# Optimization experiments

Hardware: AMD Instinct MI355X
Metric: run time of the kernel (lower is better)

## Reference

```python
import jax, jax.numpy as jnp
import numpy as np

N_NODES = 50000
N_GRAPHS = 2048
BN_EPS = 1e-5


def setup_inputs() -> dict:
    key = jax.random.key(0)
    ks = jax.random.split(key, 12)
    n_feat, dim, n_out, n_edges = 128, 128, 12, 800000
    x = jax.random.normal(ks[0], (N_NODES, n_feat), dtype=jnp.float32)
    edge_index = jax.random.randint(ks[1], (2, n_edges), 0, N_NODES, dtype=jnp.int32)
    batch = jnp.sort(jax.random.randint(ks[2], (N_NODES,), 0, N_GRAPHS, dtype=jnp.int32))
    def lin(k, fan_in, fan_out):
        bound = 1.0 / np.sqrt(fan_in)
        kw, kb = jax.random.split(k)
        W = jax.random.uniform(kw, (fan_in, fan_out), minval=-bound, maxval=bound, dtype=jnp.float32)
        b = jax.random.uniform(kb, (fan_out,), minval=-bound, maxval=bound, dtype=jnp.float32)
        return W, b
    W1, b1 = lin(ks[3], n_feat, dim)
    W2, b2 = lin(ks[4], dim, dim)
    gamma = jnp.ones((dim,), dtype=jnp.float32)
    beta = jnp.zeros((dim,), dtype=jnp.float32)
    Wf1, bf1 = lin(ks[5], dim, 2 * dim)
    Wf2, bf2 = lin(ks[6], 2 * dim, n_out)
    return {"x": x, "edge_index": edge_index, "batch": batch,
            "W1": W1, "b1": b1, "W2": W2, "b2": b2,
            "gamma": gamma, "beta": beta,
            "Wf1": Wf1, "bf1": bf1, "Wf2": Wf2, "bf2": bf2}


def reference(x, edge_index, batch, W1, b1, W2, b2, gamma, beta, Wf1, bf1, Wf2, bf2):
    src, dst = edge_index[0], edge_index[1]
    # GINConv (eps=0): h = nn1(x + sum_{j in N(i)} x_j), scatter-add at dst
    agg = jax.ops.segment_sum(x[src], dst, num_segments=N_NODES)  # [N, F]
    h = x + agg
    h = jax.nn.relu(h @ W1 + b1) @ W2 + b2  # nn1 MLP
    h = jax.nn.relu(h)
    # BatchNorm1d (training mode: batch statistics, biased variance)
    mean = jnp.mean(h, axis=0)
    var = jnp.mean((h - mean) ** 2, axis=0)
    h = (h - mean) * jax.lax.rsqrt(var + BN_EPS) * gamma + beta
    # global_add_pool over graphs
    g = jax.ops.segment_sum(h, batch, num_segments=N_GRAPHS)  # [G, dim]
    g = jax.nn.relu(g @ Wf1 + bf1)
    return g @ Wf2 + bf2  # [G, n_outputs]
```

## Files before the change

kernel.cpp:

```cpp
#include <hip/hip_runtime.h>

#define N_FEAT   128
#define N_GRAPHS 2048
#define BN_EPS   1e-5f
#define LDA      136
#define FHLD     132
#define EPB      4096

typedef __attribute__((ext_vector_type(8))) short  bf16x8;
typedef __attribute__((ext_vector_type(4))) float  f32x4;

__device__ __forceinline__ unsigned short f2bf(float f) {
    union { float f; unsigned int u; } c; c.f = f;
    unsigned int r = c.u + 0x7fffu + ((c.u >> 16) & 1u);
    return (unsigned short)(r >> 16);
}
__device__ __forceinline__ float bf2f(unsigned short h) {
    union { unsigned int u; float f; } c; c.u = ((unsigned int)h) << 16;
    return c.f;
}

__device__ __forceinline__ void acc8(float* a, int4 u) {
    unsigned int w[4] = {(unsigned int)u.x, (unsigned int)u.y,
                         (unsigned int)u.z, (unsigned int)u.w};
    #pragma unroll
    for (int k = 0; k < 4; ++k) {
        a[2 * k]     += __uint_as_float(w[k] << 16);
        a[2 * k + 1] += __uint_as_float(w[k] & 0xffff0000u);
    }
}

__global__ __launch_bounds__(256) void k_prep(const float* __restrict__ x,
                                              unsigned short* __restrict__ xb,
                                              int n8, int nbx,
                                              const float* __restrict__ W1,
                                              const float* __restrict__ W2,
                                              unsigned short* __restrict__ Wt1,
                                              unsigned short* __restrict__ Wt2,
                                              const int* __restrict__ batch,
                                              int* __restrict__ cnt, int n_nodes)
{
    int b = blockIdx.x, t = threadIdx.x;
    if (b < nbx) {
        int i = b * 256 + t;
        if (i >= n8) return;
        float4 a = ((const float4*)x)[i * 2];
        float4 c = ((const float4*)x)[i * 2 + 1];
        ushort4 u0, u1;
        u0.x = f2bf(a.x); u0.y = f2bf(a.y); u0.z = f2bf(a.z); u0.w = f2bf(a.w);
        u1.x = f2bf(c.x); u1.y = f2bf(c.y); u1.z = f2bf(c.z); u1.w = f2bf(c.w);
        ((ushort4*)xb)[i * 2]     = u0;
        ((ushort4*)xb)[i * 2 + 1] = u1;
    } else if (b < nbx + 128) {
        int i = (b - nbx) * 256 + t;
        int which = i >> 14;
        int k = (i >> 7) & 127;
        int c = i & 127;
        const float* W = which ? W2 : W1;
        unsigned short* O = which ? Wt2 : Wt1;
        O[c * 128 + k] = f2bf(W[k * 128 + c]);
    } else {
        int i = (b - nbx - 128) * 256 + t;
        if (i < n_nodes) atomicAdd(&cnt[batch[i]], 1);
    }
}

__global__ __launch_bounds__(256) void k_bhist(const int* __restrict__ dst,
                                               int* __restrict__ bcnt,
                                               int n_edges, int nb2)
{
    __shared__ int lc[256];
    int t = threadIdx.x;
    lc[t] = 0;
    __syncthreads();
    int base = blockIdx.x * EPB;
    for (int i = t; i < EPB; i += 256) {
        int e = base + i;
        if (e < n_edges) atomicAdd(&lc[dst[e] >> 8], 1);
    }
    __syncthreads();
    bcnt[t * nb2 + blockIdx.x] = lc[t];
}

__global__ __launch_bounds__(256) void k_bsum(const int* __restrict__ v,
                                              int* __restrict__ chsum, int n)
{
    __shared__ int s[256];
    int t = threadIdx.x;
    int i = blockIdx.x * 256 + t;
    s[t] = (i < n) ? v[i] : 0;
    __syncthreads();
    for (int o = 128; o > 0; o >>= 1) {
        if (t < o) s[t] += s[t + o];
        __syncthreads();
    }
    if (t == 0) chsum[blockIdx.x] = s[0];
}

__global__ __launch_bounds__(1024) void k_bscan2(const int* __restrict__ chsum,
                                                 int* __restrict__ choff, int nchunk)
{
    __shared__ int s[1024];
    int t = threadIdx.x;
    int v = (t < nchunk) ? chsum[t] : 0;
    s[t] = v;
    __syncthreads();
    for (int o = 1; o < 1024; o <<= 1) {
        int u = (t >= o) ? s[t - o] : 0;
        __syncthreads();
        s[t] += u;
        __syncthreads();
    }
    choff[t] = s[t] - v;
}

__global__ __launch_bounds__(256) void k_bapply(const int* __restrict__ v,
                                                const int* __restrict__ choff,
                                                int* __restrict__ out, int n)
{
    __shared__ int s[256];
    int t = threadIdx.x;
    int i = blockIdx.x * 256 + t;
    int c = (i < n) ? v[i] : 0;
    s[t] = c;
    __syncthreads();
    for (int o = 1; o < 256; o <<= 1) {
        int u = (t >= o) ? s[t - o] : 0;
        __syncthreads();
        s[t] += u;
        __syncthreads();
    }
    if (i < n) out[i] = choff[blockIdx.x] + s[t] - c;
}

__global__ __launch_bounds__(256) void k_part(const int* __restrict__ src,
                                              const int* __restrict__ dst,
                                              const int* __restrict__ boff2,
                                              unsigned* __restrict__ epart,
                                              int n_edges, int nb2)
{
    __shared__ int lc[256];
    __shared__ int lofs[256];
    __shared__ unsigned buf[EPB];
    int t = threadIdx.x, blk = blockIdx.x;
    int base = blk * EPB;
    lc[t] = 0;
    __syncthreads();
    for (int i = t; i < EPB; i += 256) {
        int e = base + i;
        if (e < n_edges) atomicAdd(&lc[dst[e] >> 8], 1);
    }
    __syncthreads();
    int v = lc[t];
    lofs[t] = v;
    __syncthreads();
    for (int o = 1; o < 256; o <<= 1) {
        int u = (t >= o) ? lofs[t - o] : 0;
        __syncthreads();
        lofs[t] += u;
        __syncthreads();
    }
    int excl = lofs[t] - v;
    __syncthreads();
    lofs[t] = excl;
    lc[t] = 0;
    __syncthreads();
    for (int i = t; i < EPB; i += 256) {
        int e = base + i;
        if (e < n_edges) {
            int d = dst[e];
            int b = d >> 8;
            unsigned pack = ((unsigned)d << 16) | (unsigned)src[e];
            int r = atomicAdd(&lc[b], 1);
            buf[lofs[b] + r] = pack;
        }
    }
    __syncthreads();
    int total = min(EPB, n_edges - base);
    for (int i = t; i < total; i += 256) {
        unsigned pack = buf[i];
        int b = pack >> 24;
        int gpos = boff2[b * nb2 + blk] + (i - lofs[b]);
        epart[gpos] = pack;
    }
}

__global__ __launch_bounds__(256) void k_bfill(const unsigned* __restrict__ epart,
                                               const int* __restrict__ boff2,
                                               int* __restrict__ row_start,
                                               unsigned short* __restrict__ csr,
                                               int n_nodes, int nb2, int nbkt)
{
    __shared__ int cur[256];
    __shared__ int sc2[256];
    __shared__ unsigned short seg[8192];
    int t = threadIdx.x, b = blockIdx.x;
    int node0 = b * 256;
    int nodes = min(256, n_nodes - node0);
    int ebeg = boff2[(size_t)b * nb2];
    int eend = (b + 1 < nbkt) ? boff2[(size_t)(b + 1) * nb2] : boff2[(size_t)nbkt * nb2];

    cur[t] = 0;
    __syncthreads();
    for (int i = ebeg + t; i < eend; i += 256)
        atomicAdd(&cur[(epart[i] >> 16) - node0], 1);
    __syncthreads();
    int v = cur[t];
    sc2[t] = v;
    __syncthreads();
    for (int o = 1; o < 256; o <<= 1) {
        int u = (t >= o) ? sc2[t - o] : 0;
        __syncthreads();
        sc2[t] += u;
        __syncthreads();
    }
    int excl = sc2[t] - v;
    if (t < nodes) row_start[node0 + t] = ebeg + excl;
    if (b == nbkt - 1 && t == 0) row_start[n_nodes] = eend;
    __syncthreads();
    cur[t] = excl;
    __syncthreads();
    for (int i = ebeg + t; i < eend; i += 256) {
        unsigned pack = epart[i];
        int idx = (pack >> 16) - node0;
        int slot = atomicAdd(&cur[idx], 1);
        seg[slot] = (unsigned short)(pack & 0xffffu);
    }
    __syncthreads();
    int seglen = eend - ebeg;
    for (int i = t; i < seglen; i += 256) csr[ebeg + i] = seg[i];
}

__global__ __launch_bounds__(256) void k_gather(const float* __restrict__ x,
                                                const unsigned short* __restrict__ xb,
                                                const unsigned short* __restrict__ csr,
                                                const int* __restrict__ row_start,
                                                unsigned short* __restrict__ Ahi,
                                                unsigned short* __restrict__ Alo,
                                                int n_nodes)
{
    int node = blockIdx.x * 4 + (threadIdx.x >> 6);
    if (node >= n_nodes) return;
    int l = threadIdx.x & 63;
    int q = l >> 4;
    int lq = l & 15;
    const int4* xb4 = (const int4*)xb;
    int beg = row_start[node], end = row_start[node + 1];
    float a[8];
    #pragma unroll
    for (int i = 0; i < 8; ++i) a[i] = 0.f;

    int j = beg + q;
    for (; j + 4 < end; j += 8) {
        int s0 = csr[j], s1 = csr[j + 4];
        int4 u0 = xb4[(size_t)s0 * 16 + lq];
        int4 u1 = xb4[(size_t)s1 * 16 + lq];
        acc8(a, u0);
        acc8(a, u1);
    }
    for (; j < end; j += 4) {
        int4 u = xb4[(size_t)csr[j] * 16 + lq];
        acc8(a, u);
    }
    #pragma unroll
    for (int i = 0; i < 8; ++i) {
        a[i] += __shfl_xor(a[i], 16);
        a[i] += __shfl_xor(a[i], 32);
    }
    if (q == 0) {
        float4 s0 = ((const float4*)(x + (size_t)node * 128))[lq * 2];
        float4 s1 = ((const float4*)(x + (size_t)node * 128))[lq * 2 + 1];
        a[0] += s0.x; a[1] += s0.y; a[2] += s0.z; a[3] += s0.w;
        a[4] += s1.x; a[5] += s1.y; a[6] += s1.z; a[7] += s1.w;
        unsigned int hw[4], lw[4];
        #pragma unroll
        for (int i = 0; i < 4; ++i) {
            unsigned short h0 = f2bf(a[2 * i]);
            unsigned short h1 = f2bf(a[2 * i + 1]);
            unsigned short l0 = f2bf(a[2 * i] - bf2f(h0));
            unsigned short l1 = f2bf(a[2 * i + 1] - bf2f(h1));
            hw[i] = (unsigned int)h0 | ((unsigned int)h1 << 16);
            lw[i] = (unsigned int)l0 | ((unsigned int)l1 << 16);
        }
        int4 hv = make_int4(hw[0], hw[1], hw[2], hw[3]);
        int4 lv = make_int4(lw[0], lw[1], lw[2], lw[3]);
        *(int4*)(Ahi + (size_t)node * 128 + lq * 8) = hv;
        *(int4*)(Alo + (size_t)node * 128 + lq * 8) = lv;
    }
}

__global__ __launch_bounds__(256) void k_mlp1_mfma(const unsigned short* __restrict__ Ahi,
                                                   const unsigned short* __restrict__ Alo,
                                                   const unsigned short* __restrict__ Wt1,
                                                   const float* __restrict__ b1,
                                                   const unsigned short* __restrict__ Wt2,
                                                   const float* __restrict__ b2,
                                                   const int* __restrict__ batch,
                                                   float* __restrict__ g_raw,
                                                   float* __restrict__ partial,
                                                   int n_rows)
{
    __shared__ __align__(16) char smem[64 * LDA * 2 * sizeof(unsigned short)];
    unsigned short* sHi = (unsigned short*)smem;
    unsigned short* sLo = sHi + 64 * LDA;

    int t = threadIdx.x;
    int wave = t >> 6, l = t & 63;
    int lr = l & 15;
    int lk = l >> 4;
    int row0 = blockIdx.x * 64;
    int col0 = wave * 32;

    #pragma unroll
    for (int it = 0; it < 4; ++it) {
        int idx = it * 256 + t;
        int r = idx >> 4, c8 = idx & 15;
        int gr = row0 + r;
        int4 vh = make_int4(0, 0, 0, 0), vl = make_int4(0, 0, 0, 0);
        if (gr < n_rows) {
            vh = ((const int4*)(Ahi + (size_t)gr * 128))[c8];
            vl = ((const int4*)(Alo + (size_t)gr * 128))[c8];
        }
        *(int4*)&sHi[r * LDA + c8 * 8] = vh;
        *(int4*)&sLo[r * LDA + c8 * 8] = vl;
    }
    __syncthreads();

    f32x4 acc[4][2];
    #pragma unroll
    for (int m = 0; m < 4; ++m)
        #pragma unroll
        for (int n = 0; n < 2; ++n) acc[m][n] = (f32x4){0.f, 0.f, 0.f, 0.f};

    #pragma unroll
    for (int ks = 0; ks < 4; ++ks) {
        bf16x8 bfrag[2];
        #pragma unroll
        for (int n = 0; n < 2; ++n) {
            int c = col0 + n * 16 + lr;
            bfrag[n] = *(const bf16x8*)(Wt1 + (size_t)c * 128 + ks * 32 + lk * 8);
        }
        #pragma unroll
        for (int m = 0; m < 4; ++m) {
            bf16x8 ah = *(const bf16x8*)&sHi[(m * 16 + lr) * LDA + ks * 32 + lk * 8];
            bf16x8 al = *(const bf16x8*)&sLo[(m * 16 + lr) * LDA + ks * 32 + lk * 8];
            #pragma unroll
            for (int n = 0; n < 2; ++n) {
                acc[m][n] = __builtin_amdgcn_mfma_f32_16x16x32_bf16(ah, bfrag[n], acc[m][n], 0, 0, 0);
                acc[m][n] = __builtin_amdgcn_mfma_f32_16x16x32_bf16(al, bfrag[n], acc[m][n], 0, 0, 0);
            }
        }
    }
    __syncthreads();

    #pragma unroll
    for (int n = 0; n < 2; ++n) {
        int c = col0 + n * 16 + lr;
        float bb = b1[c];
        #pragma unroll
        for (int m = 0; m < 4; ++m) {
            #pragma unroll
            for (int i = 0; i < 4; ++i) {
                int r = m * 16 + lk * 4 + i;
                float v = fmaxf(acc[m][n][i] + bb, 0.f);
                unsigned short hb = f2bf(v);
                sHi[r * LDA + c] = hb;
                sLo[r * LDA + c] = f2bf(v - bf2f(hb));
            }
        }
    }
    __syncthreads();

    #pragma unroll
    for (int m = 0; m < 4; ++m)
        #pragma unroll
        for (int n = 0; n < 2; ++n) acc[m][n] = (f32x4){0.f, 0.f, 0.f, 0.f};

    #pragma unroll
    for (int ks = 0; ks < 4; ++ks) {
        bf16x8 bfrag[2];
        #pragma unroll
        for (int n = 0; n < 2; ++n) {
            int c = col0 + n * 16 + lr;
            bfrag[n] = *(const bf16x8*)(Wt2 + (size_t)c * 128 + ks * 32 + lk * 8);
        }
        #pragma unroll
        for (int m = 0; m < 4; ++m) {
            bf16x8 ah = *(const bf16x8*)&sHi[(m * 16 + lr) * LDA + ks * 32 + lk * 8];
            bf16x8 al = *(const bf16x8*)&sLo[(m * 16 + lr) * LDA + ks * 32 + lk * 8];
            #pragma unroll
            for (int n = 0; n < 2; ++n) {
                acc[m][n] = __builtin_amdgcn_mfma_f32_16x16x32_bf16(ah, bfrag[n], acc[m][n], 0, 0, 0);
                acc[m][n] = __builtin_amdgcn_mfma_f32_16x16x32_bf16(al, bfrag[n], acc[m][n], 0, 0, 0);
            }
        }
    }

    float bb0 = b2[col0 + lr];
    float bb1 = b2[col0 + 16 + lr];
    int c0 = col0 + lr, c1 = col0 + 16 + lr;
    float v0s[4][4], v1s[4][4];
    float ps[2] = {0.f, 0.f}, pq[2] = {0.f, 0.f};
    #pragma unroll
    for (int m = 0; m < 4; ++m) {
        #pragma unroll
        for (int i = 0; i < 4; ++i) {
            int gr = row0 + m * 16 + lk * 4 + i;
            float v0 = fmaxf(acc[m][0][i] + bb0, 0.f);
            float v1 = fmaxf(acc[m][1][i] + bb1, 0.f);
            if (gr >= n_rows) { v0 = 0.f; v1 = 0.f; }
            v0s[m][i] = v0; v1s[m][i] = v1;
            ps[0] += v0; pq[0] += v0 * v0;
            ps[1] += v1; pq[1] += v1 * v1;
        }
    }
    #pragma unroll
    for (int n = 0; n < 2; ++n) {
        ps[n] += __shfl_xor(ps[n], 16); ps[n] += __shfl_xor(ps[n], 32);
        pq[n] += __shfl_xor(pq[n], 16); pq[n] += __shfl_xor(pq[n], 32);
    }
    if (lk == 0) {
        partial[(size_t)blockIdx.x * 256 + c0]       = ps[0];
        partial[(size_t)blockIdx.x * 256 + c1]       = ps[1];
        partial[(size_t)blockIdx.x * 256 + 128 + c0] = pq[0];
        partial[(size_t)blockIdx.x * 256 + 128 + c1] = pq[1];
    }

    __syncthreads();
    float (*fH)[FHLD] = (float (*)[FHLD])smem;
    int* sB = (int*)(smem + 64 * FHLD * sizeof(float));
    if (t < 64) sB[t] = (row0 + t < n_rows) ? batch[row0 + t] : -1;
    #pragma unroll
    for (int m = 0; m < 4; ++m) {
        #pragma unroll
        for (int i = 0; i < 4; ++i) {
            int r = m * 16 + lk * 4 + i;
            fH[r][c0] = v0s[m][i];
            fH[r][c1] = v1s[m][i];
        }
    }
    __syncthreads();

    {
        int c = t & 127;
        int rbeg = (t >> 7) * 32, rend = rbeg + 32;
        float a = 0.f;
        int bcur = sB[rbeg];
        for (int r = rbeg; r < rend; ++r) {
            int b = sB[r];
            if (b != bcur) {
                if (bcur >= 0) unsafeAtomicAdd(&g_raw[(size_t)bcur * 128 + c], a);
                a = 0.f; bcur = b;
            }
            a += fH[r][c];
        }
        if (bcur >= 0) unsafeAtomicAdd(&g_raw[(size_t)bcur * 128 + c], a);
    }
}

__global__ __launch_bounds__(256) void k_bnred(const float* __restrict__ partial,
                                               float* __restrict__ stats, int nblk)
{
    int j = threadIdx.x;
    float s = 0.f;
    for (int b = blockIdx.x; b < nblk; b += gridDim.x)
        s += partial[(size_t)b * 256 + j];
    unsafeAtomicAdd(&stats[j], s);
}

__global__ __launch_bounds__(256) void k_head(const float* __restrict__ g_raw,
                                              const int* __restrict__ cnt,
                                              const float* __restrict__ stats,
                                              const float* __restrict__ gamma,
                                              const float* __restrict__ beta,
                                              const float* __restrict__ Wf1,
                                              const float* __restrict__ bf1,
                                              const float* __restrict__ Wf2,
                                              const float* __restrict__ bf2,
                                              float* __restrict__ out, int n_rows)
{
    __shared__ float sg[128];
    __shared__ float sh[256];
    int t = threadIdx.x;
    int G = blockIdx.x;
    if (t < 128) {
        float inv_n = 1.0f / (float)n_rows;
        float mean = stats[t] * inv_n;
        float var = stats[128 + t] * inv_n - mean * mean;
        float inv = rsqrtf(var + BN_EPS);
        float scale = gamma[t] * inv;
        float shift = beta[t] - mean * scale;
        float c = (float)cnt[G];
        sg[t] = g_raw[(size_t)G * 128 + t] * scale + c * shift;
    }
    __syncthreads();
    float a = bf1[t];
    #pragma unroll 8
    for (int k = 0; k < 128; ++k) a = fmaf(sg[k], Wf1[k * 256 + t], a);
    sh[t] = fmaxf(a, 0.f);
    __syncthreads();
    if (t < 192) {
        int o = t >> 4, l = t & 15;
        float p = 0.f;
        for (int k = l; k < 256; k += 16) p += sh[k] * Wf2[k * 12 + o];
        #pragma unroll
        for (int m = 8; m >= 1; m >>= 1) p += __shfl_xor(p, m, 16);
        if (l == 0) out[(size_t)G * 12 + o] = p + bf2[o];
    }
}

extern "C" void kernel_launch(void* const* d_in, const int* in_sizes, int n_in,
                              void* d_out, int out_size, void* d_ws, size_t ws_size,
                              hipStream_t stream)
{
    const float* x     = (const float*)d_in[0];
    const int*   ei    = (const int*)d_in[1];
    const int*   batch = (const int*)d_in[2];
    const float* W1    = (const float*)d_in[3];
    const float* b1    = (const float*)d_in[4];
    const float* W2    = (const float*)d_in[5];
    const float* b2    = (const float*)d_in[6];
    const float* gamma = (const float*)d_in[7];
    const float* beta  = (const float*)d_in[8];
    const float* Wf1   = (const float*)d_in[9];
    const float* bf1   = (const float*)d_in[10];
    const float* Wf2   = (const float*)d_in[11];
    const float* bf2   = (const float*)d_in[12];

    int n_nodes = in_sizes[0] / N_FEAT;
    int n_edges = in_sizes[1] / 2;
    const int* src = ei;
    const int* dst = ei + n_edges;

    char* ws = (char*)d_ws;
    size_t planeBytes = (size_t)n_nodes * N_FEAT * sizeof(unsigned short);
    size_t gBytes     = (size_t)N_GRAPHS * N_FEAT * sizeof(float);
    int nblk_m = (n_nodes + 63) / 64;
    int nb2    = (n_edges + EPB - 1) / EPB;
    int nbkt   = (n_nodes + 255) / 256;
    int nscan  = 256 * nb2;
    int nchunk = (nscan + 255) / 256;

    unsigned short* Ahi = (unsigned short*)ws;
    unsigned short* Alo = (unsigned short*)(ws + planeBytes);
    unsigned short* xb  = (unsigned short*)(ws + 2 * planeBytes);
    float* g_raw = (float*)(ws + 3 * planeBytes);
    float* stats = (float*)((char*)g_raw + gBytes);
    float* sc    = stats + 256;
    int*   cnt   = (int*)(sc + 256);
    unsigned short* Wt1 = (unsigned short*)(cnt + N_GRAPHS);
    unsigned short* Wt2 = Wt1 + 128 * 128;
    float* partial = (float*)(Wt2 + 128 * 128);
    char* p = (char*)(partial + (size_t)nblk_m * 256);
    int* row_start = (int*)p;   p += (size_t)(n_nodes + 1) * sizeof(int);
    int* bcnt      = (int*)p;   p += (size_t)nscan * sizeof(int);
    int* bch       = (int*)p;   p += 1024 * sizeof(int);
    int* bchoff    = (int*)p;   p += 1024 * sizeof(int);
    int* boff2     = (int*)p;   p += (size_t)nscan * sizeof(int);
    unsigned* epart = (unsigned*)p;  p += (size_t)n_edges * sizeof(unsigned);
    unsigned short* csr = (unsigned short*)p;

    hipMemsetAsync(g_raw, 0, gBytes + (256 + 256 + N_GRAPHS) * sizeof(float), stream);

    int n8 = n_nodes * N_FEAT / 8;
    int nbx = (n8 + 255) / 256;
    int nbg = (n_nodes + 255) / 256;
    k_prep<<<nbx + 128 + nbg, 256, 0, stream>>>(x, xb, n8, nbx, W1, W2, Wt1, Wt2,
                                                batch, cnt, n_nodes);

    k_bhist<<<nb2, 256, 0, stream>>>(dst, bcnt, n_edges, nb2);
    k_bsum<<<nchunk, 256, 0, stream>>>(bcnt, bch, nscan);
    k_bscan2<<<1, 1024, 0, stream>>>(bch, bchoff, nchunk);
    k_bapply<<<nchunk, 256, 0, stream>>>(bcnt, bchoff, boff2, nscan);
    k_part<<<nb2, 256, 0, stream>>>(src, dst, boff2, epart, n_edges, nb2);
    k_bfill<<<nbkt, 256, 0, stream>>>(epart, boff2, row_start, csr, n_nodes, nb2, nbkt);

    k_gather<<<(n_nodes + 3) / 4, 256, 0, stream>>>(x, xb, csr, row_start, Ahi, Alo, n_nodes);

    k_mlp1_mfma<<<nblk_m, 256, 0, stream>>>(Ahi, Alo, Wt1, b1, Wt2, b2, batch,
                                            g_raw, partial, n_nodes);

    k_bnred<<<64, 256, 0, stream>>>(partial, stats, nblk_m);
    k_head<<<N_GRAPHS, 256, 0, stream>>>(g_raw, cnt, stats, gamma, beta,
                                         Wf1, bf1, Wf2, bf2, (float*)d_out, n_nodes);
}
```

Before: 135.9 us.

## Drop bf16 hi/lo split in MLP and fuse bucket scan into two kernels

The MLP stage no longer splits activations into high and low bf16 planes. It keeps one bf16 plane, which halves the MFMA count, the LDS traffic and the gather stores. The three-kernel bucket prefix scan becomes per-bucket totals accumulated atomically in the histogram kernel plus a single scan kernel, removing two launches. The precision loss on activations could push the output beyond tolerance, and the new scan assumes nb2 is at most 256.

New measurement: 129.8 us. 1.05x faster.

```diff
diff --git a/kernel.cpp b/kernel.cpp
--- a/kernel.cpp
+++ b/kernel.cpp
@@ -67,6 +67,7 @@
 
 __global__ __launch_bounds__(256) void k_bhist(const int* __restrict__ dst,
                                                int* __restrict__ bcnt,
+                                               int* __restrict__ btot,
                                                int n_edges, int nb2)
 {
     __shared__ int lc[256];
@@ -80,48 +81,24 @@
     }
     __syncthreads();
     bcnt[t * nb2 + blockIdx.x] = lc[t];
-}
-
-__global__ __launch_bounds__(256) void k_bsum(const int* __restrict__ v,
-                                              int* __restrict__ chsum, int n)
+    if (lc[t]) atomicAdd(&btot[t], lc[t]);
+}
+
+__global__ __launch_bounds__(256) void k_bscan3(const int* __restrict__ bcnt,
+                                                const int* __restrict__ btot,
+                                                int* __restrict__ boff2, int nb2)
 {
     __shared__ int s[256];
-    int t = threadIdx.x;
-    int i = blockIdx.x * 256 + t;
-    s[t] = (i < n) ? v[i] : 0;
+    int t = threadIdx.x, b = blockIdx.x;
+    s[t] = (t < b) ? btot[t] : 0;
     __syncthreads();
     for (int o = 128; o > 0; o >>= 1) {
         if (t < o) s[t] += s[t + o];
         __syncthreads();
     }
-    if (t == 0) chsum[blockIdx.x] = s[0];
-}
-
-__global__ __launch_bounds__(1024) void k_bscan2(const int* __restrict__ chsum,
-                                                 int* __restrict__ choff, int nchunk)
-{
-    __shared__ int s[1024];
-    int t = threadIdx.x;
-    int v = (t < nchunk) ? chsum[t] : 0;
-    s[t] = v;
-    __syncthreads();
-    for (int o = 1; o < 1024; o <<= 1) {
-        int u = (t >= o) ? s[t - o] : 0;
-        __syncthreads();
-        s[t] += u;
-        __syncthreads();
-    }
-    choff[t] = s[t] - v;
-}
-
-__global__ __launch_bounds__(256) void k_bapply(const int* __restrict__ v,
-                                                const int* __restrict__ choff,
-                                                int* __restrict__ out, int n)
-{
-    __shared__ int s[256];
-    int t = threadIdx.x;
-    int i = blockIdx.x * 256 + t;
-    int c = (i < n) ? v[i] : 0;
+    int base = s[0];
+    __syncthreads();
+    int c = (t < nb2) ? bcnt[b * nb2 + t] : 0;
     s[t] = c;
     __syncthreads();
     for (int o = 1; o < 256; o <<= 1) {
@@ -130,7 +107,7 @@
         s[t] += u;
         __syncthreads();
     }
-    if (i < n) out[i] = choff[blockIdx.x] + s[t] - c;
+    if (t < nb2) boff2[b * nb2 + t] = base + s[t] - c;
 }
 
 __global__ __launch_bounds__(256) void k_part(const int* __restrict__ src,
@@ -235,8 +212,7 @@
                                                 const unsigned short* __restrict__ xb,
                                                 const unsigned short* __restrict__ csr,
                                                 const int* __restrict__ row_start,
-                                                unsigned short* __restrict__ Ahi,
-                                                unsigned short* __restrict__ Alo,
+                                                unsigned short* __restrict__ A,
                                                 int n_nodes)
 {
     int node = blockIdx.x * 4 + (threadIdx.x >> 6);
@@ -272,25 +248,18 @@
         float4 s1 = ((const float4*)(x + (size_t)node * 128))[lq * 2 + 1];
         a[0] += s0.x; a[1] += s0.y; a[2] += s0.z; a[3] += s0.w;
         a[4] += s1.x; a[5] += s1.y; a[6] += s1.z; a[7] += s1.w;
-        unsigned int hw[4], lw[4];
+        unsigned int hw[4];
         #pragma unroll
         for (int i = 0; i < 4; ++i) {
             unsigned short h0 = f2bf(a[2 * i]);
             unsigned short h1 = f2bf(a[2 * i + 1]);
-            unsigned short l0 = f2bf(a[2 * i] - bf2f(h0));
-            unsigned short l1 = f2bf(a[2 * i + 1] - bf2f(h1));
             hw[i] = (unsigned int)h0 | ((unsigned int)h1 << 16);
-            lw[i] = (unsigned int)l0 | ((unsigned int)l1 << 16);
-        }
-        int4 hv = make_int4(hw[0], hw[1], hw[2], hw[3]);
-        int4 lv = make_int4(lw[0], lw[1], lw[2], lw[3]);
-        *(int4*)(Ahi + (size_t)node * 128 + lq * 8) = hv;
-        *(int4*)(Alo + (size_t)node * 128 + lq * 8) = lv;
-    }
-}
-
-__global__ __launch_bounds__(256) void k_mlp1_mfma(const unsigned short* __restrict__ Ahi,
-                                                   const unsigned short* __restrict__ Alo,
+        }
+        *(int4*)(A + (size_t)node * 128 + lq * 8) = make_int4(hw[0], hw[1], hw[2], hw[3]);
+    }
+}
+
+__global__ __launch_bounds__(256) void k_mlp1_mfma(const unsigned short* __restrict__ A,
                                                    const unsigned short* __restrict__ Wt1,
                                                    const float* __restrict__ b1,
                                                    const unsigned short* __restrict__ Wt2,
@@ -300,9 +269,8 @@
                                                    float* __restrict__ partial,
                                                    int n_rows)
 {
-    __shared__ __align__(16) char smem[64 * LDA * 2 * sizeof(unsigned short)];
-    unsigned short* sHi = (unsigned short*)smem;
-    unsigned short* sLo = sHi + 64 * LDA;
+    __shared__ __align__(16) char smem[64 * FHLD * 4 + 256];
+    unsigned short* sA = (unsigned short*)smem;
 
     int t = threadIdx.x;
     int wave = t >> 6, l = t & 63;
@@ -316,13 +284,9 @@
         int idx = it * 256 + t;
         int r = idx >> 4, c8 = idx & 15;
         int gr = row0 + r;
-        int4 vh = make_int4(0, 0, 0, 0), vl = make_int4(0, 0, 0, 0);
-        if (gr < n_rows) {
-            vh = ((const int4*)(Ahi + (size_t)gr * 128))[c8];
-            vl = ((const int4*)(Alo + (size_t)gr * 128))[c8];
-        }
-        *(int4*)&sHi[r * LDA + c8 * 8] = vh;
-        *(int4*)&sLo[r * LDA + c8 * 8] = vl;
+        int4 vh = make_int4(0, 0, 0, 0);
+        if (gr < n_rows) vh = ((const int4*)(A + (size_t)gr * 128))[c8];
+        *(int4*)&sA[r * LDA + c8 * 8] = vh;
     }
     __syncthreads();
 
@@ -342,13 +306,10 @@
         }
         #pragma unroll
         for (int m = 0; m < 4; ++m) {
-            bf16x8 ah = *(const bf16x8*)&sHi[(m * 16 + lr) * LDA + ks * 32 + lk * 8];
-            bf16x8 al = *(const bf16x8*)&sLo[(m * 16 + lr) * LDA + ks * 32 + lk * 8];
+            bf16x8 ah = *(const bf16x8*)&sA[(m * 16 + lr) * LDA + ks * 32 + lk * 8];
             #pragma unroll
-            for (int n = 0; n < 2; ++n) {
+            for (int n = 0; n < 2; ++n)
                 acc[m][n] = __builtin_amdgcn_mfma_f32_16x16x32_bf16(ah, bfrag[n], acc[m][n], 0, 0, 0);
-                acc[m][n] = __builtin_amdgcn_mfma_f32_16x16x32_bf16(al, bfrag[n], acc[m][n], 0, 0, 0);
-            }
         }
     }
     __syncthreads();
@@ -362,10 +323,7 @@
             #pragma unroll
             for (int i = 0; i < 4; ++i) {
                 int r = m * 16 + lk * 4 + i;
-                float v = fmaxf(acc[m][n][i] + bb, 0.f);
-                unsigned short hb = f2bf(v);
-                sHi[r * LDA + c] = hb;
-                sLo[r * LDA + c] = f2bf(v - bf2f(hb));
+                sA[r * LDA + c] = f2bf(fmaxf(acc[m][n][i] + bb, 0.f));
             }
         }
     }
@@ -386,13 +344,10 @@
         }
         #pragma unroll
         for (int m = 0; m < 4; ++m) {
-            bf16x8 ah = *(const bf16x8*)&sHi[(m * 16 + lr) * LDA + ks * 32 + lk * 8];
-            bf16x8 al = *(const bf16x8*)&sLo[(m * 16 + lr) * LDA + ks * 32 + lk * 8];
+            bf16x8 ah = *(const bf16x8*)&sA[(m * 16 + lr) * LDA + ks * 32 + lk * 8];
             #pragma unroll
-            for (int n = 0; n < 2; ++n) {
+            for (int n = 0; n < 2; ++n)
                 acc[m][n] = __builtin_amdgcn_mfma_f32_16x16x32_bf16(ah, bfrag[n], acc[m][n], 0, 0, 0);
-                acc[m][n] = __builtin_amdgcn_mfma_f32_16x16x32_bf16(al, bfrag[n], acc[m][n], 0, 0, 0);
-            }
         }
     }
 
@@ -539,28 +494,25 @@
     int nb2    = (n_edges + EPB - 1) / EPB;
     int nbkt   = (n_nodes + 255) / 256;
     int nscan  = 256 * nb2;
-    int nchunk = (nscan + 255) / 256;
-
-    unsigned short* Ahi = (unsigned short*)ws;
-    unsigned short* Alo = (unsigned short*)(ws + planeBytes);
-    unsigned short* xb  = (unsigned short*)(ws + 2 * planeBytes);
-    float* g_raw = (float*)(ws + 3 * planeBytes);
+
+    unsigned short* A   = (unsigned short*)ws;
+    unsigned short* xb  = (unsigned short*)(ws + planeBytes);
+    float* g_raw = (float*)(ws + 2 * planeBytes);
     float* stats = (float*)((char*)g_raw + gBytes);
-    float* sc    = stats + 256;
-    int*   cnt   = (int*)(sc + 256);
-    unsigned short* Wt1 = (unsigned short*)(cnt + N_GRAPHS);
+    float* scSp  = stats + 256;
+    int*   cnt   = (int*)(scSp + 256);
+    int*   btot  = cnt + N_GRAPHS;
+    unsigned short* Wt1 = (unsigned short*)(btot + 256);
     unsigned short* Wt2 = Wt1 + 128 * 128;
     float* partial = (float*)(Wt2 + 128 * 128);
     char* p = (char*)(partial + (size_t)nblk_m * 256);
     int* row_start = (int*)p;   p += (size_t)(n_nodes + 1) * sizeof(int);
     int* bcnt      = (int*)p;   p += (size_t)nscan * sizeof(int);
-    int* bch       = (int*)p;   p += 1024 * sizeof(int);
-    int* bchoff    = (int*)p;   p += 1024 * sizeof(int);
     int* boff2     = (int*)p;   p += (size_t)nscan * sizeof(int);
     unsigned* epart = (unsigned*)p;  p += (size_t)n_edges * sizeof(unsigned);
     unsigned short* csr = (unsigned short*)p;
 
-    hipMemsetAsync(g_raw, 0, gBytes + (256 + 256 + N_GRAPHS) * sizeof(float), stream);
+    hipMemsetAsync(g_raw, 0, gBytes + (256 + 256 + N_GRAPHS + 256) * sizeof(float), stream);
 
     int n8 = n_nodes * N_FEAT / 8;
     int nbx = (n8 + 255) / 256;
@@ -568,16 +520,14 @@
     k_prep<<<nbx + 128 + nbg, 256, 0, stream>>>(x, xb, n8, nbx, W1, W2, Wt1, Wt2,
                                                 batch, cnt, n_nodes);
 
-    k_bhist<<<nb2, 256, 0, stream>>>(dst, bcnt, n_edges, nb2);
-    k_bsum<<<nchunk, 256, 0, stream>>>(bcnt, bch, nscan);
-    k_bscan2<<<1, 1024, 0, stream>>>(bch, bchoff, nchunk);
-    k_bapply<<<nchunk, 256, 0, stream>>>(bcnt, bchoff, boff2, nscan);
+    k_bhist<<<nb2, 256, 0, stream>>>(dst, bcnt, btot, n_edges, nb2);
+    k_bscan3<<<256, 256, 0, stream>>>(bcnt, btot, boff2, nb2);
     k_part<<<nb2, 256, 0, stream>>>(src, dst, boff2, epart, n_edges, nb2);
     k_bfill<<<nbkt, 256, 0, stream>>>(epart, boff2, row_start, csr, n_nodes, nb2, nbkt);
 
-    k_gather<<<(n_nodes + 3) / 4, 256, 0, stream>>>(x, xb, csr, row_start, Ahi, Alo, n_nodes);
-
-    k_mlp1_mfma<<<nblk_m, 256, 0, stream>>>(Ahi, Alo, Wt1, b1, Wt2, b2, batch,
+    k_gather<<<(n_nodes + 3) / 4, 256, 0, stream>>>(x, xb, csr, row_start, A, n_nodes);
+
+    k_mlp1_mfma<<<nblk_m, 256, 0, stream>>>(A, Wt1, b1, Wt2, b2, batch,
                                             g_raw, partial, n_nodes);
 
     k_bnred<<<64, 256, 0, stream>>>(partial, stats, nblk_m);
```
